# Optimization experiments

Hardware: AMD Instinct MI355X
Metric: run time of the kernel (lower is better)

Reference implementation:

```python
import jax, jax.numpy as jnp
import numpy as np

D_MODEL = 256; D_STATE = 128; EXPAND = 2; HEADDIM = 64
D_INNER = EXPAND * D_MODEL            # 512
NHEADS = D_INNER // HEADDIM           # 8
CONV_DIM = D_INNER + 2 * D_STATE      # 768
D_IN_PROJ = 2 * D_INNER + 2 * D_STATE + NHEADS  # 1288
KCONV = 4
BATCH = 16; SEQ = 1024; CHUNK = 64
EPS = 1e-5


def setup_inputs() -> dict:
    key = jax.random.key(0)
    ks = jax.random.split(key, 8)
    # dt_bias = inverse-softplus of dt ~ U[1e-3, 1e-1] (Mamba2 init)
    dt = jnp.exp(jax.random.uniform(ks[3], (NHEADS,), jnp.float32,
                                    np.log(1e-3), np.log(1e-1)))
    dt_bias = dt + jnp.log(-jnp.expm1(-dt))
    return {
        "u": jax.random.normal(ks[0], (BATCH, SEQ, D_MODEL), jnp.float32),
        "W_in": 0.02 * jax.random.normal(ks[1], (D_MODEL, D_IN_PROJ), jnp.float32),
        "conv_w": 0.2 * jax.random.normal(ks[2], (CONV_DIM, KCONV), jnp.float32),
        "conv_b": jnp.zeros((CONV_DIM,), jnp.float32),
        "dt_bias": dt_bias,
        "A_log": jnp.log(jax.random.uniform(ks[4], (NHEADS,), jnp.float32, 1.0, 16.0)),
        "D": jnp.ones((NHEADS,), jnp.float32),
        "norm_w": jnp.ones((D_INNER,), jnp.float32),
        "W_out": 0.02 * jax.random.normal(ks[5], (D_INNER, D_MODEL), jnp.float32),
    }


def _segsum(x):
    # x: (..., L) -> (..., L, L) lower-triangular cumulative segment sums
    L = x.shape[-1]
    c = jnp.cumsum(x, axis=-1)
    ss = c[..., :, None] - c[..., None, :]
    mask = jnp.tril(jnp.ones((L, L), bool))
    return jnp.where(mask, ss, -jnp.inf)


def _ssd(X, A, Bm, Cm, chunk):
    # Chunked SSD selective scan (Mamba2, ngroups=1).
    # X:(b,t,h,p)  A:(b,t,h)  Bm,Cm:(b,t,n)
    b, t, h, p = X.shape
    nc = t // chunk
    X = X.reshape(b, nc, chunk, h, p)
    A = A.reshape(b, nc, chunk, h).transpose(0, 3, 1, 2)   # (b,h,c,l)
    Bm = Bm.reshape(b, nc, chunk, -1)
    Cm = Cm.reshape(b, nc, chunk, -1)
    A_cs = jnp.cumsum(A, axis=-1)                          # (b,h,c,l)
    Lmat = jnp.exp(_segsum(A))                             # (b,h,c,l,l)
    # within-chunk (diagonal) contribution
    Y_diag = jnp.einsum('bcln,bcsn,bhcls,bcshp->bclhp', Cm, Bm, Lmat, X)
    # per-chunk end states
    decay_states = jnp.exp(A_cs[..., -1:] - A_cs)          # (b,h,c,l)
    states = jnp.einsum('bcln,bhcl,bclhp->bchpn', Bm, decay_states, X)
    # inter-chunk recurrence (vectorized over chunks)
    A_chunk = jnp.pad(A_cs[..., -1], ((0, 0), (0, 0), (1, 0)))
    decay_chunk = jnp.exp(_segsum(A_chunk))                # (b,h,c+1,c+1)
    states = jnp.concatenate([jnp.zeros_like(states[:, :1]), states], axis=1)
    new_states = jnp.einsum('bhzc,bchpn->bzhpn', decay_chunk, states)
    states = new_states[:, :-1]                            # state entering each chunk
    Y_off = jnp.einsum('bcln,bchpn,bhcl->bclhp', Cm, states, jnp.exp(A_cs))
    return (Y_diag + Y_off).reshape(b, t, h, p)


def reference(u, W_in, conv_w, conv_b, dt_bias, A_log, D, norm_w, W_out):
    B, T, _ = u.shape
    zxbcdt = u @ W_in                                      # (B,T,1288)
    z, xBC, dt = jnp.split(zxbcdt, [D_INNER, D_INNER + CONV_DIM], axis=-1)
    # causal depthwise conv1d, kernel KCONV
    xp = jnp.pad(xBC, ((0, 0), (KCONV - 1, 0), (0, 0)))
    kern = conv_w.T[:, None, :]                            # (K,1,C)
    xBC = jax.lax.conv_general_dilated(
        xp, kern, (1,), 'VALID',
        dimension_numbers=('NWC', 'WIO', 'NWC'), feature_group_count=CONV_DIM)
    xBC = jax.nn.silu(xBC + conv_b)
    x, Bc, Cc = jnp.split(xBC, [D_INNER, D_INNER + D_STATE], axis=-1)
    x = x.reshape(B, T, NHEADS, HEADDIM)
    dt = jax.nn.softplus(dt + dt_bias)                     # (B,T,H)
    A = -jnp.exp(A_log)                                    # (H,)
    y = _ssd(x * dt[..., None], dt * A, Bc, Cc, CHUNK)     # (B,T,H,P)
    y = y + D[:, None] * x                                 # skip term
    y = y.reshape(B, T, D_INNER)
    # gated RMSNorm: norm(y * silu(z)) * weight
    g = y * jax.nn.silu(z)
    g = g * jax.lax.rsqrt(jnp.mean(g * g, axis=-1, keepdims=True) + EPS) * norm_w
    return g @ W_out
```

## Files before the change

### kernel.cpp

```cpp
#include <hip/hip_runtime.h>
#include <hip/hip_bf16.h>
#include <math.h>

#define BATCHN  16
#define SEQ     1024
#define DMODEL  256
#define DSTATE  128
#define HEADDIM 64
#define DINNER  512
#define NHEADS  8
#define CONVDIM 768
#define DINPROJ 1288
#define ZXLD    1280
#define KCONV   4
#define NCHUNK  16
#define LCHUNK  64
#define EPSV    1e-5f
#define ROWS    (BATCHN*SEQ)

typedef __attribute__((ext_vector_type(8))) __bf16 bf16x8;
typedef __attribute__((ext_vector_type(4))) float  f32x4;

__device__ inline ushort f2bf(float f) {
    union { float f; uint32_t u; } v; v.f = f;
    uint32_t r = v.u + 0x7fff + ((v.u >> 16) & 1);
    return (ushort)(r >> 16);
}
__device__ inline float bf2f(ushort u) {
    union { uint32_t u; float f; } v; v.u = ((uint32_t)u) << 16;
    return v.f;
}

__global__ __launch_bounds__(256) void transpose_cast2_k(const float* __restrict__ W_in,
                                                         const float* __restrict__ W_out,
                                                         ushort* __restrict__ WtA,
                                                         ushort* __restrict__ WtB) {
    __shared__ float Ts[32][33];
    int bid = blockIdx.x;
    const float* src; ushort* dst; int K, ldsrc, nx;
    if (bid < 320) { src = W_in;  dst = WtA; K = DMODEL; ldsrc = DINPROJ; nx = 40; }
    else { bid -= 320; src = W_out; dst = WtB; K = DINNER; ldsrc = DMODEL; nx = 8; }
    const int n0 = (bid % nx) * 32, k0 = (bid / nx) * 32;
    const int tx = threadIdx.x & 31, ty = threadIdx.x >> 5;
    #pragma unroll
    for (int j = 0; j < 4; ++j) {
        int kl = ty * 4 + j;
        Ts[kl][tx] = src[(size_t)(k0 + kl) * ldsrc + n0 + tx];
    }
    __syncthreads();
    #pragma unroll
    for (int j = 0; j < 4; ++j) {
        int nl = ty * 4 + j;
        dst[(size_t)(n0 + nl) * K + k0 + tx] = f2bf(Ts[tx][nl]);
    }
}

__global__ __launch_bounds__(256) void dt_cast_k(const float* __restrict__ u,
                                                 const float* __restrict__ W_in,
                                                 const float* __restrict__ dt_bias,
                                                 const float* __restrict__ A_log,
                                                 ushort* __restrict__ ubf,
                                                 float* __restrict__ dtb,
                                                 float* __restrict__ adtb) {
    __shared__ float Uld[32][264];
    __shared__ float Ws[DMODEL][NHEADS];
    const int tid = threadIdx.x;
    #pragma unroll
    for (int j = 0; j < 8; ++j) {
        int idx = tid + j * 256;
        Ws[idx >> 3][idx & 7] = W_in[(size_t)(idx >> 3) * DINPROJ + 1280 + (idx & 7)];
    }
    const int row0 = blockIdx.x * 32;
    #pragma unroll
    for (int v = 0; v < 8; ++v) {
        int e = v * 1024 + tid * 4;
        int r = e >> 8, cc = e & 255;
        float4 x = *(const float4*)&u[(size_t)(row0 + r) * DMODEL + cc];
        *(float4*)&Uld[r][cc] = x;
        ushort t4[4];
        t4[0]=f2bf(x.x); t4[1]=f2bf(x.y); t4[2]=f2bf(x.z); t4[3]=f2bf(x.w);
        *(ushort4*)&ubf[(size_t)(row0 + r) * DMODEL + cc] = *(ushort4*)t4;
    }
    __syncthreads();
    const int row = tid >> 3, h = tid & 7;
    float acc = 0.f;
    #pragma unroll 8
    for (int k = 0; k < DMODEL; k += 4) {
        float4 uv = *(const float4*)&Uld[row][k];
        acc += uv.x * Ws[k][h] + uv.y * Ws[k+1][h] + uv.z * Ws[k+2][h] + uv.w * Ws[k+3][h];
    }
    float v = acc + dt_bias[h];
    float dt = (v > 20.f) ? v : log1pf(__expf(v));
    dtb [(size_t)(row0 + row) * NHEADS + h] = dt;
    adtb[(size_t)(row0 + row) * NHEADS + h] = dt * (-__expf(A_log[h]));
}

#define LDSW 72
template<typename CT>
__global__ __launch_bounds__(256) void gemm_bf16(const ushort* __restrict__ A,
                                                 const ushort* __restrict__ Bt,
                                                 CT* __restrict__ C,
                                                 int M, int N, int K, int nx) {
    __shared__ ushort As[128 * LDSW];
    __shared__ ushort Bs[128 * LDSW];
    const int tid  = threadIdx.x;
    const int nwg  = gridDim.x;
    const int work = (blockIdx.x & 7) * (nwg >> 3) + (blockIdx.x >> 3);
    const int m0 = (work / nx) * 128, n0 = (work % nx) * 128;
    const int wid = tid >> 6, lane = tid & 63;
    const int wr = wid >> 1, wc = wid & 1;
    const int r = tid >> 1, kq = tid & 1;
    const int fr = lane & 15, kc = lane >> 4;

    f32x4 acc[4][4];
    #pragma unroll
    for (int i = 0; i < 4; ++i)
        #pragma unroll
        for (int j = 0; j < 4; ++j) acc[i][j] = (f32x4)0.f;

    for (int kt = 0; kt < K; kt += 64) {
        const ushort* ap = &A [(size_t)(m0 + r) * K + kt + kq * 32];
        const ushort* bp = &Bt[(size_t)(n0 + r) * K + kt + kq * 32];
        #pragma unroll
        for (int v = 0; v < 4; ++v) {
            *(uint4*)&As[r * LDSW + kq * 32 + v * 8] = *(const uint4*)(ap + v * 8);
            *(uint4*)&Bs[r * LDSW + kq * 32 + v * 8] = *(const uint4*)(bp + v * 8);
        }
        __syncthreads();
        #pragma unroll
        for (int kk = 0; kk < 2; ++kk) {
            bf16x8 af[4], bfv[4];
            #pragma unroll
            for (int i = 0; i < 4; ++i) {
                af[i]  = *(const bf16x8*)&As[(wr * 64 + i * 16 + fr) * LDSW + kk * 32 + kc * 8];
                bfv[i] = *(const bf16x8*)&Bs[(wc * 64 + i * 16 + fr) * LDSW + kk * 32 + kc * 8];
            }
            #pragma unroll
            for (int i = 0; i < 4; ++i)
                #pragma unroll
                for (int j = 0; j < 4; ++j)
                    acc[i][j] = __builtin_amdgcn_mfma_f32_16x16x32_bf16(af[i], bfv[j], acc[i][j], 0, 0, 0);
        }
        __syncthreads();
    }
    #pragma unroll
    for (int i = 0; i < 4; ++i)
        #pragma unroll
        for (int j = 0; j < 4; ++j)
            #pragma unroll
            for (int q = 0; q < 4; ++q) {
                int rr = m0 + wr * 64 + i * 16 + (lane >> 4) * 4 + q;
                int cc = n0 + wc * 64 + j * 16 + (lane & 15);
                if constexpr (sizeof(CT) == 4) C[(size_t)rr * N + cc] = acc[i][j][q];
                else                           C[(size_t)rr * N + cc] = f2bf(acc[i][j][q]);
            }
}

__global__ __launch_bounds__(256) void conv_silu_k(const ushort* __restrict__ zx,
                                                   const float* __restrict__ cw,
                                                   const float* __restrict__ cb,
                                                   ushort* __restrict__ out) {
    __shared__ float cws[KCONV][CONVDIM];
    __shared__ float cbs[CONVDIM];
    const int tid = threadIdx.x;
    #pragma unroll
    for (int it = 0; it < 3; ++it) {
        int i = tid + it * 256;
        cbs[i] = cb[i];
        #pragma unroll
        for (int k = 0; k < KCONV; ++k) cws[k][i] = cw[i * KCONV + k];
    }
    __syncthreads();

    const int idx = blockIdx.x * 256 + tid;
    const int cg = idx % 96, btq = idx / 96;
    const int c0 = cg * 8;
    const int bt0 = btq * 4;
    const int t0 = bt0 & (SEQ - 1);

    float wv[KCONV][8], bias[8];
    #pragma unroll
    for (int j = 0; j < 8; ++j) bias[j] = cbs[c0 + j];
    #pragma unroll
    for (int k = 0; k < KCONV; ++k) {
        float4 a = *(const float4*)&cws[k][c0];
        float4 b = *(const float4*)&cws[k][c0 + 4];
        wv[k][0] = a.x; wv[k][1] = a.y; wv[k][2] = a.z; wv[k][3] = a.w;
        wv[k][4] = b.x; wv[k][5] = b.y; wv[k][6] = b.z; wv[k][7] = b.w;
    }
    float xr[7][8];
    #pragma unroll
    for (int r = 0; r < 7; ++r) {
        int tt = t0 - 3 + r;
        if (tt >= 0) {
            uint4 v = *(const uint4*)&zx[(size_t)(bt0 - 3 + r) * ZXLD + DINNER + c0];
            const ushort* pv = (const ushort*)&v;
            #pragma unroll
            for (int j = 0; j < 8; ++j) xr[r][j] = bf2f(pv[j]);
        } else {
            #pragma unroll
            for (int j = 0; j < 8; ++j) xr[r][j] = 0.f;
        }
    }
    #pragma unroll
    for (int dt = 0; dt < 4; ++dt) {
        float acc[8];
        #pragma unroll
        for (int j = 0; j < 8; ++j) acc[j] = bias[j];
        #pragma unroll
        for (int k = 0; k < KCONV; ++k)
            #pragma unroll
            for (int j = 0; j < 8; ++j) acc[j] += xr[dt + k][j] * wv[k][j];
        ushort res[8];
        #pragma unroll
        for (int j = 0; j < 8; ++j)
            res[j] = f2bf(acc[j] / (1.f + __expf(-acc[j])));
        *(uint4*)&out[(size_t)(bt0 + dt) * CONVDIM + c0] = *(uint4*)res;
    }
}

#define SLDA 136
#define SLDB 72
__global__ __launch_bounds__(256) void ssd_mfma_k(const ushort* __restrict__ xbc,
                                                  const float* __restrict__ dtb,
                                                  const float* __restrict__ adtb,
                                                  const float* __restrict__ Dp,
                                                  ushort* __restrict__ ybuf,
                                                  ushort* __restrict__ states,
                                                  float* __restrict__ acsbuf,
                                                  float* __restrict__ chunksum) {
    const int c = blockIdx.x, b = blockIdx.y, hgrp = blockIdx.z;
    const int row0 = b * SEQ + c * LCHUNK;
    const int tid = threadIdx.x;
    const int lane = tid & 63, w = tid >> 6;
    const int fr = lane & 15, kc = lane >> 4;

    __shared__ union {
        struct { ushort Bs[64][SLDA]; ushort Cs[64][SLDA]; } p1;
        struct { ushort Ps[64][SLDB]; ushort Xt[64][SLDB]; ushort Xdt[64][SLDB]; } p2;
    } U;
    __shared__ ushort Btr[128][SLDB];
    __shared__ float acs4[4][64];
    __shared__ float dts[4][64];
    __shared__ float decs[4][64];

    {
        const int hh = hgrp * 4 + w;
        float v = adtb[(size_t)(row0 + lane) * NHEADS + hh];
        #pragma unroll
        for (int off = 1; off < 64; off <<= 1) {
            float t = __shfl_up(v, off);
            if (lane >= off) v += t;
        }
        acs4[w][lane] = v;
        float tot = __shfl(v, 63);
        decs[w][lane] = __expf(tot - v);
        acsbuf[(((size_t)b * NCHUNK + c) * NHEADS + hh) * LCHUNK + lane] = v;
        if (lane == 63) chunksum[((size_t)b * NCHUNK + c) * NHEADS + hh] = v;
        dts[w][lane] = dtb[(size_t)(row0 + lane) * NHEADS + hh];
    }
    for (int it = 0; it < 4; ++it) {
        int idx = tid + it * 256;
        int l = idx >> 4, ng = idx & 15;
        const ushort* rp = &xbc[(size_t)(row0 + l) * CONVDIM + DINNER];
        uint4 vb = *(const uint4*)(rp + ng * 8);
        *(uint4*)&U.p1.Bs[l][ng * 8] = vb;
        uint4 vc = *(const uint4*)(rp + DSTATE + ng * 8);
        *(uint4*)&U.p1.Cs[l][ng * 8] = vc;
        const ushort* pv = (const ushort*)&vb;
        #pragma unroll
        for (int j = 0; j < 8; ++j) Btr[ng * 8 + j][l] = pv[j];
    }
    __syncthreads();

    const int wr = w >> 1, wc = w & 1;
    f32x4 accG[2][2];
    #pragma unroll
    for (int i = 0; i < 2; ++i)
        #pragma unroll
        for (int j = 0; j < 2; ++j) accG[i][j] = (f32x4)0.f;
    #pragma unroll
    for (int kt = 0; kt < 4; ++kt) {
        bf16x8 af[2], bfv[2];
        #pragma unroll
        for (int i = 0; i < 2; ++i) af[i]  = *(const bf16x8*)&U.p1.Cs[wr*32 + i*16 + fr][kt*32 + kc*8];
        #pragma unroll
        for (int j = 0; j < 2; ++j) bfv[j] = *(const bf16x8*)&U.p1.Bs[wc*32 + j*16 + fr][kt*32 + kc*8];
        #pragma unroll
        for (int i = 0; i < 2; ++i)
            #pragma unroll
            for (int j = 0; j < 2; ++j)
                accG[i][j] = __builtin_amdgcn_mfma_f32_16x16x32_bf16(af[i], bfv[j], accG[i][j], 0, 0, 0);
    }
    __syncthreads();

    for (int hl = 0; hl < 4; ++hl) {
        const int hh = hgrp * 4 + hl;
        {
            const int p = lane;
            ushort xt[16], xdt[16];
            #pragma unroll
            for (int j = 0; j < 16; ++j) {
                int l = w * 16 + j;
                float xv = bf2f(xbc[(size_t)(row0 + l) * CONVDIM + hh * HEADDIM + p])
                           * dts[hl][l];
                xt[j]  = f2bf(xv);
                xdt[j] = f2bf(xv * decs[hl][l]);
            }
            #pragma unroll
            for (int v = 0; v < 4; ++v) {
                *(ushort4*)&U.p2.Xt [p][w*16 + v*4] = *(ushort4*)&xt[v*4];
                *(ushort4*)&U.p2.Xdt[p][w*16 + v*4] = *(ushort4*)&xdt[v*4];
            }
        }
        #pragma unroll
        for (int i = 0; i < 2; ++i)
            #pragma unroll
            for (int j = 0; j < 2; ++j)
                #pragma unroll
                for (int q = 0; q < 4; ++q) {
                    int l = wr*32 + i*16 + (lane >> 4)*4 + q;
                    int s = wc*32 + j*16 + fr;
                    float v = 0.f;
                    if (s < l)       v = accG[i][j][q] * __expf(acs4[hl][l] - acs4[hl][s]);
                    else if (s == l) v = accG[i][j][q] + Dp[hh] / dts[hl][l];
                    U.p2.Ps[l][s] = f2bf(v);
                }
        __syncthreads();
        {
            f32x4 acc[4];
            #pragma unroll
            for (int j = 0; j < 4; ++j) acc[j] = (f32x4)0.f;
            #pragma unroll
            for (int kt = 0; kt < 2; ++kt) {
                bf16x8 af = *(const bf16x8*)&U.p2.Ps[w*16 + fr][kt*32 + kc*8];
                #pragma unroll
                for (int j = 0; j < 4; ++j) {
                    bf16x8 bfv = *(const bf16x8*)&U.p2.Xt[j*16 + fr][kt*32 + kc*8];
                    acc[j] = __builtin_amdgcn_mfma_f32_16x16x32_bf16(af, bfv, acc[j], 0, 0, 0);
                }
            }
            #pragma unroll
            for (int j = 0; j < 4; ++j)
                #pragma unroll
                for (int q = 0; q < 4; ++q) {
                    int l = w*16 + (lane >> 4)*4 + q;
                    int p = j*16 + fr;
                    ybuf[(size_t)(row0 + l) * DINNER + hh * HEADDIM + p] = f2bf(acc[j][q]);
                }
        }
        {
            f32x4 acc2[4][2];
            #pragma unroll
            for (int mt = 0; mt < 4; ++mt)
                #pragma unroll
                for (int jt = 0; jt < 2; ++jt) acc2[mt][jt] = (f32x4)0.f;
            #pragma unroll
            for (int kt = 0; kt < 2; ++kt) {
                bf16x8 a4[4], b2[2];
                #pragma unroll
                for (int mt = 0; mt < 4; ++mt) a4[mt] = *(const bf16x8*)&U.p2.Xdt[mt*16 + fr][kt*32 + kc*8];
                #pragma unroll
                for (int jt = 0; jt < 2; ++jt) b2[jt] = *(const bf16x8*)&Btr[w*32 + jt*16 + fr][kt*32 + kc*8];
                #pragma unroll
                for (int mt = 0; mt < 4; ++mt)
                    #pragma unroll
                    for (int jt = 0; jt < 2; ++jt)
                        acc2[mt][jt] = __builtin_amdgcn_mfma_f32_16x16x32_bf16(a4[mt], b2[jt], acc2[mt][jt], 0, 0, 0);
            }
            ushort* sb = states + ((((size_t)b * NCHUNK + c) * NHEADS + hh) * HEADDIM) * DSTATE;
            #pragma unroll
            for (int mt = 0; mt < 4; ++mt)
                #pragma unroll
                for (int jt = 0; jt < 2; ++jt)
                    #pragma unroll
                    for (int q = 0; q < 4; ++q) {
                        int p = mt*16 + (lane >> 4)*4 + q;
                        int n = w*32 + jt*16 + fr;
                        sb[(size_t)p * DSTATE + n] = f2bf(acc2[mt][jt][q]);
                    }
        }
        __syncthreads();
    }
}

__global__ __launch_bounds__(256) void scan_k(ushort* __restrict__ states,
                                              const float* __restrict__ chunksum) {
    const int bid = blockIdx.x;
    const int pq = bid & 3, h = (bid >> 2) & 7, b = bid >> 5;
    const int tid = threadIdx.x;
    float pref[8];
    #pragma unroll
    for (int k = 0; k < 8; ++k) pref[k] = 0.f;
    for (int c = 0; c < NCHUNK; ++c) {
        ushort* base = states + (((size_t)b * NCHUNK + c) * NHEADS + h) * (HEADDIM * DSTATE)
                       + pq * 2048 + tid * 8;
        float dec = __expf(chunksum[((size_t)b * NCHUNK + c) * NHEADS + h]);
        uint4 v = *(const uint4*)base;
        const ushort* pv = (const ushort*)&v;
        ushort outv[8];
        #pragma unroll
        for (int j = 0; j < 8; ++j) {
            float cur = bf2f(pv[j]);
            outv[j] = f2bf(pref[j]);
            pref[j] = dec * pref[j] + cur;
        }
        *(uint4*)base = *(uint4*)outv;
    }
}

#define YLDS 520
__global__ __launch_bounds__(256) void yoff_gate_k(const ushort* __restrict__ xbc,
                                                   const ushort* __restrict__ states,
                                                   const float* __restrict__ acsbuf,
                                                   const ushort* __restrict__ ybuf,
                                                   const ushort* __restrict__ zx,
                                                   const float* __restrict__ nw,
                                                   ushort* __restrict__ gbuf) {
    const int c = blockIdx.x, b = blockIdx.y;
    const int row0 = b * SEQ + c * LCHUNK;
    const int tid = threadIdx.x;
    const int lane = tid & 63, w = tid >> 6;
    const int fr = lane & 15, kc = lane >> 4;
    __shared__ ushort Csh[64][SLDA];
    __shared__ ushort Ssh[64][SLDA];
    __shared__ ushort Ys[64][YLDS];
    __shared__ float eah[64];

    for (int it = 0; it < 4; ++it) {
        int idx = tid + it * 256;
        int l = idx >> 4, ng = idx & 15;
        *(uint4*)&Csh[l][ng * 8] =
            *(const uint4*)&xbc[(size_t)(row0 + l) * CONVDIM + DINNER + DSTATE + ng * 8];
    }
    for (int hl = 0; hl < NHEADS; ++hl) {
        __syncthreads();
        const ushort* sb = states + ((((size_t)b * NCHUNK + c) * NHEADS + hl) * HEADDIM) * DSTATE;
        for (int it = 0; it < 4; ++it) {
            int idx = tid + it * 256;
            int p = idx >> 4, ng = idx & 15;
            *(uint4*)&Ssh[p][ng * 8] = *(const uint4*)&sb[(size_t)p * DSTATE + ng * 8];
        }
        if (tid < 64)
            eah[tid] = __expf(acsbuf[(((size_t)b * NCHUNK + c) * NHEADS + hl) * LCHUNK + tid]);
        __syncthreads();
        f32x4 acc[4];
        #pragma unroll
        for (int j = 0; j < 4; ++j) acc[j] = (f32x4)0.f;
        #pragma unroll
        for (int kt = 0; kt < 4; ++kt) {
            bf16x8 af = *(const bf16x8*)&Csh[w*16 + fr][kt*32 + kc*8];
            #pragma unroll
            for (int j = 0; j < 4; ++j) {
                bf16x8 bfv = *(const bf16x8*)&Ssh[j*16 + fr][kt*32 + kc*8];
                acc[j] = __builtin_amdgcn_mfma_f32_16x16x32_bf16(af, bfv, acc[j], 0, 0, 0);
            }
        }
        #pragma unroll
        for (int j = 0; j < 4; ++j)
            #pragma unroll
            for (int q = 0; q < 4; ++q) {
                int l = w*16 + (lane >> 4)*4 + q;
                int p = j*16 + fr;
                float val = bf2f(ybuf[(size_t)(row0 + l) * DINNER + hl * HEADDIM + p])
                            + acc[j][q] * eah[l];
                Ys[l][hl * HEADDIM + p] = f2bf(val);
            }
    }
    __syncthreads();
    float nwv[8];
    #pragma unroll
    for (int j = 0; j < 8; ++j) nwv[j] = nw[lane * 8 + j];
    for (int i = 0; i < 16; ++i) {
        int l = w * 16 + i;
        int row = row0 + l;
        uint4 zv = *(const uint4*)&zx[(size_t)row * ZXLD + lane * 8];
        const ushort* pz = (const ushort*)&zv;
        float g[8], ss = 0.f;
        #pragma unroll
        for (int j = 0; j < 8; ++j) {
            float y = bf2f(Ys[l][lane * 8 + j]);
            float z = bf2f(pz[j]);
            float sz = z / (1.f + __expf(-z));
            g[j] = y * sz;
            ss += g[j] * g[j];
        }
        #pragma unroll
        for (int off = 32; off; off >>= 1) ss += __shfl_xor(ss, off);
        float r = rsqrtf(ss / (float)DINNER + EPSV);
        ushort res[8];
        #pragma unroll
        for (int j = 0; j < 8; ++j) res[j] = f2bf(g[j] * r * nwv[j]);
        *(uint4*)&gbuf[(size_t)row * DINNER + lane * 8] = *(uint4*)res;
    }
}

extern "C" void kernel_launch(void* const* d_in, const int* in_sizes, int n_in,
                              void* d_out, int out_size, void* d_ws, size_t ws_size,
                              hipStream_t stream) {
    const float* u       = (const float*)d_in[0];
    const float* W_in    = (const float*)d_in[1];
    const float* conv_w  = (const float*)d_in[2];
    const float* conv_b  = (const float*)d_in[3];
    const float* dt_bias = (const float*)d_in[4];
    const float* A_log   = (const float*)d_in[5];
    const float* Dp      = (const float*)d_in[6];
    const float* norm_w  = (const float*)d_in[7];
    const float* W_out   = (const float*)d_in[8];
    float* out = (float*)d_out;

    char* p = (char*)d_ws;
    ushort* zx       = (ushort*)p; p += (size_t)ROWS * ZXLD * sizeof(ushort);
    ushort* ybuf     = (ushort*)p; p += (size_t)ROWS * DINNER * sizeof(ushort);
    ushort* gbuf     = (ushort*)p; p += (size_t)ROWS * DINNER * sizeof(ushort);
    ushort* states   = (ushort*)p; p += (size_t)BATCHN * NCHUNK * NHEADS * HEADDIM * DSTATE * sizeof(ushort);
    ushort* xbc      = (ushort*)p; p += (size_t)ROWS * CONVDIM * sizeof(ushort);
    ushort* ubf      = (ushort*)p; p += (size_t)ROWS * DMODEL * sizeof(ushort);
    float*  dtb      = (float*)p;  p += (size_t)ROWS * NHEADS  * sizeof(float);
    float*  adtb     = (float*)p;  p += (size_t)ROWS * NHEADS  * sizeof(float);
    float*  chunksum = (float*)p;  p += (size_t)BATCHN * NCHUNK * NHEADS * sizeof(float);
    float*  acsbuf   = (float*)p;  p += (size_t)BATCHN * NCHUNK * NHEADS * LCHUNK * sizeof(float);
    ushort* WtA      = (ushort*)p; p += (size_t)ZXLD * DMODEL * sizeof(ushort);
    ushort* WtB      = (ushort*)p; p += (size_t)DMODEL * DINNER * sizeof(ushort);

    dt_cast_k<<<ROWS/32, 256, 0, stream>>>(u, W_in, dt_bias, A_log, ubf, dtb, adtb);
    transpose_cast2_k<<<448, 256, 0, stream>>>(W_in, W_out, WtA, WtB);
    gemm_bf16<ushort><<<(ZXLD/128)*(ROWS/128), 256, 0, stream>>>(
        ubf, WtA, zx, ROWS, ZXLD, DMODEL, ZXLD/128);
    conv_silu_k<<<(ROWS/4)*96/256, 256, 0, stream>>>(zx, conv_w, conv_b, xbc);
    ssd_mfma_k<<<dim3(NCHUNK, BATCHN, 2), 256, 0, stream>>>(
        xbc, dtb, adtb, Dp, ybuf, states, acsbuf, chunksum);
    scan_k<<<BATCHN*NHEADS*4, 256, 0, stream>>>(states, chunksum);
    yoff_gate_k<<<dim3(NCHUNK, BATCHN), 256, 0, stream>>>(
        xbc, states, acsbuf, ybuf, zx, norm_w, gbuf);
    gemm_bf16<float><<<(DMODEL/128)*(ROWS/128), 256, 0, stream>>>(
        gbuf, WtB, out, ROWS, DMODEL, DINNER, DMODEL/128);
}
```

Before: 131.4 us.

## Fuse SSD chunk, inter-chunk scan, and state-output into one sequential-chunk kernel

```diff
diff --git a/kernel.cpp b/kernel.cpp
--- a/kernel.cpp
+++ b/kernel.cpp
@@ -221,278 +221,175 @@
 
 #define SLDA 136
 #define SLDB 72
-__global__ __launch_bounds__(256) void ssd_mfma_k(const ushort* __restrict__ xbc,
-                                                  const float* __restrict__ dtb,
-                                                  const float* __restrict__ adtb,
-                                                  const float* __restrict__ Dp,
-                                                  ushort* __restrict__ ybuf,
-                                                  ushort* __restrict__ states,
-                                                  float* __restrict__ acsbuf,
-                                                  float* __restrict__ chunksum) {
-    const int c = blockIdx.x, b = blockIdx.y, hgrp = blockIdx.z;
-    const int row0 = b * SEQ + c * LCHUNK;
+__global__ __launch_bounds__(512) void ssd_fused_k(const ushort* __restrict__ xbc,
+                                                   const float* __restrict__ dtb,
+                                                   const float* __restrict__ adtb,
+                                                   const float* __restrict__ Dp,
+                                                   ushort* __restrict__ ybuf) {
+    const int ph = blockIdx.x, h = blockIdx.y, b = blockIdx.z;
+    const int p0 = ph * 32;
     const int tid = threadIdx.x;
     const int lane = tid & 63, w = tid >> 6;
     const int fr = lane & 15, kc = lane >> 4;
 
-    __shared__ union {
-        struct { ushort Bs[64][SLDA]; ushort Cs[64][SLDA]; } p1;
-        struct { ushort Ps[64][SLDB]; ushort Xt[64][SLDB]; ushort Xdt[64][SLDB]; } p2;
-    } U;
+    __shared__ ushort Bsh[64][SLDA];
+    __shared__ ushort Csh[64][SLDA];
     __shared__ ushort Btr[128][SLDB];
-    __shared__ float acs4[4][64];
-    __shared__ float dts[4][64];
-    __shared__ float decs[4][64];
-
-    {
-        const int hh = hgrp * 4 + w;
-        float v = adtb[(size_t)(row0 + lane) * NHEADS + hh];
-        #pragma unroll
-        for (int off = 1; off < 64; off <<= 1) {
-            float t = __shfl_up(v, off);
-            if (lane >= off) v += t;
-        }
-        acs4[w][lane] = v;
-        float tot = __shfl(v, 63);
-        decs[w][lane] = __expf(tot - v);
-        acsbuf[(((size_t)b * NCHUNK + c) * NHEADS + hh) * LCHUNK + lane] = v;
-        if (lane == 63) chunksum[((size_t)b * NCHUNK + c) * NHEADS + hh] = v;
-        dts[w][lane] = dtb[(size_t)(row0 + lane) * NHEADS + hh];
-    }
-    for (int it = 0; it < 4; ++it) {
-        int idx = tid + it * 256;
-        int l = idx >> 4, ng = idx & 15;
-        const ushort* rp = &xbc[(size_t)(row0 + l) * CONVDIM + DINNER];
-        uint4 vb = *(const uint4*)(rp + ng * 8);
-        *(uint4*)&U.p1.Bs[l][ng * 8] = vb;
-        uint4 vc = *(const uint4*)(rp + DSTATE + ng * 8);
-        *(uint4*)&U.p1.Cs[l][ng * 8] = vc;
-        const ushort* pv = (const ushort*)&vb;
-        #pragma unroll
-        for (int j = 0; j < 8; ++j) Btr[ng * 8 + j][l] = pv[j];
-    }
+    __shared__ ushort Ps [64][SLDB];
+    __shared__ ushort Xt [32][SLDB];
+    __shared__ ushort Xdt[32][SLDB];
+    __shared__ ushort Spl[32][SLDA];
+    __shared__ float acs_s[64], dts_s[64], decs_s[64];
+
+    const float Dh = Dp[h];
+    { int p = tid >> 4, ng = tid & 15;
+      uint4 z; z.x = z.y = z.z = z.w = 0u;
+      *(uint4*)&Spl[p][ng * 8] = z; }
+    const int mt = w & 1, nt0 = (w >> 1) * 2;
+    f32x4 Sp[2];
+    Sp[0] = (f32x4)0.f; Sp[1] = (f32x4)0.f;
     __syncthreads();
 
-    const int wr = w >> 1, wc = w & 1;
-    f32x4 accG[2][2];
-    #pragma unroll
-    for (int i = 0; i < 2; ++i)
-        #pragma unroll
-        for (int j = 0; j < 2; ++j) accG[i][j] = (f32x4)0.f;
-    #pragma unroll
-    for (int kt = 0; kt < 4; ++kt) {
-        bf16x8 af[2], bfv[2];
-        #pragma unroll
-        for (int i = 0; i < 2; ++i) af[i]  = *(const bf16x8*)&U.p1.Cs[wr*32 + i*16 + fr][kt*32 + kc*8];
-        #pragma unroll
-        for (int j = 0; j < 2; ++j) bfv[j] = *(const bf16x8*)&U.p1.Bs[wc*32 + j*16 + fr][kt*32 + kc*8];
-        #pragma unroll
-        for (int i = 0; i < 2; ++i)
-            #pragma unroll
-            for (int j = 0; j < 2; ++j)
-                accG[i][j] = __builtin_amdgcn_mfma_f32_16x16x32_bf16(af[i], bfv[j], accG[i][j], 0, 0, 0);
-    }
-    __syncthreads();
-
-    for (int hl = 0; hl < 4; ++hl) {
-        const int hh = hgrp * 4 + hl;
-        {
-            const int p = lane;
-            ushort xt[16], xdt[16];
-            #pragma unroll
-            for (int j = 0; j < 16; ++j) {
-                int l = w * 16 + j;
-                float xv = bf2f(xbc[(size_t)(row0 + l) * CONVDIM + hh * HEADDIM + p])
-                           * dts[hl][l];
-                xt[j]  = f2bf(xv);
-                xdt[j] = f2bf(xv * decs[hl][l]);
-            }
-            #pragma unroll
-            for (int v = 0; v < 4; ++v) {
-                *(ushort4*)&U.p2.Xt [p][w*16 + v*4] = *(ushort4*)&xt[v*4];
-                *(ushort4*)&U.p2.Xdt[p][w*16 + v*4] = *(ushort4*)&xdt[v*4];
-            }
-        }
-        #pragma unroll
-        for (int i = 0; i < 2; ++i)
-            #pragma unroll
-            for (int j = 0; j < 2; ++j)
-                #pragma unroll
-                for (int q = 0; q < 4; ++q) {
-                    int l = wr*32 + i*16 + (lane >> 4)*4 + q;
-                    int s = wc*32 + j*16 + fr;
-                    float v = 0.f;
-                    if (s < l)       v = accG[i][j][q] * __expf(acs4[hl][l] - acs4[hl][s]);
-                    else if (s == l) v = accG[i][j][q] + Dp[hh] / dts[hl][l];
-                    U.p2.Ps[l][s] = f2bf(v);
-                }
+    for (int c = 0; c < NCHUNK; ++c) {
+        const int row0 = b * SEQ + c * LCHUNK;
+        if (w == 0) {
+            float v = adtb[(size_t)(row0 + lane) * NHEADS + h];
+            #pragma unroll
+            for (int off = 1; off < 64; off <<= 1) {
+                float t = __shfl_up(v, off);
+                if (lane >= off) v += t;
+            }
+            acs_s[lane] = v;
+            float tot = __shfl(v, 63);
+            decs_s[lane] = __expf(tot - v);
+            dts_s[lane] = dtb[(size_t)(row0 + lane) * NHEADS + h];
+        }
+        #pragma unroll
+        for (int it = 0; it < 2; ++it) {
+            int idx = tid + it * 512;
+            int l = idx >> 4, ng = idx & 15;
+            const ushort* rp = &xbc[(size_t)(row0 + l) * CONVDIM + DINNER];
+            uint4 vb = *(const uint4*)(rp + ng * 8);
+            *(uint4*)&Bsh[l][ng * 8] = vb;
+            uint4 vc = *(const uint4*)(rp + DSTATE + ng * 8);
+            *(uint4*)&Csh[l][ng * 8] = vc;
+            const ushort* pv = (const ushort*)&vb;
+            #pragma unroll
+            for (int j = 0; j < 8; ++j) Btr[ng * 8 + j][l] = pv[j];
+        }
         __syncthreads();
-        {
-            f32x4 acc[4];
-            #pragma unroll
-            for (int j = 0; j < 4; ++j) acc[j] = (f32x4)0.f;
-            #pragma unroll
-            for (int kt = 0; kt < 2; ++kt) {
-                bf16x8 af = *(const bf16x8*)&U.p2.Ps[w*16 + fr][kt*32 + kc*8];
-                #pragma unroll
-                for (int j = 0; j < 4; ++j) {
-                    bf16x8 bfv = *(const bf16x8*)&U.p2.Xt[j*16 + fr][kt*32 + kc*8];
-                    acc[j] = __builtin_amdgcn_mfma_f32_16x16x32_bf16(af, bfv, acc[j], 0, 0, 0);
-                }
-            }
-            #pragma unroll
-            for (int j = 0; j < 4; ++j)
-                #pragma unroll
-                for (int q = 0; q < 4; ++q) {
-                    int l = w*16 + (lane >> 4)*4 + q;
-                    int p = j*16 + fr;
-                    ybuf[(size_t)(row0 + l) * DINNER + hh * HEADDIM + p] = f2bf(acc[j][q]);
-                }
-        }
-        {
-            f32x4 acc2[4][2];
-            #pragma unroll
-            for (int mt = 0; mt < 4; ++mt)
-                #pragma unroll
-                for (int jt = 0; jt < 2; ++jt) acc2[mt][jt] = (f32x4)0.f;
-            #pragma unroll
-            for (int kt = 0; kt < 2; ++kt) {
-                bf16x8 a4[4], b2[2];
-                #pragma unroll
-                for (int mt = 0; mt < 4; ++mt) a4[mt] = *(const bf16x8*)&U.p2.Xdt[mt*16 + fr][kt*32 + kc*8];
-                #pragma unroll
-                for (int jt = 0; jt < 2; ++jt) b2[jt] = *(const bf16x8*)&Btr[w*32 + jt*16 + fr][kt*32 + kc*8];
-                #pragma unroll
-                for (int mt = 0; mt < 4; ++mt)
-                    #pragma unroll
-                    for (int jt = 0; jt < 2; ++jt)
-                        acc2[mt][jt] = __builtin_amdgcn_mfma_f32_16x16x32_bf16(a4[mt], b2[jt], acc2[mt][jt], 0, 0, 0);
-            }
-            ushort* sb = states + ((((size_t)b * NCHUNK + c) * NHEADS + hh) * HEADDIM) * DSTATE;
-            #pragma unroll
-            for (int mt = 0; mt < 4; ++mt)
-                #pragma unroll
-                for (int jt = 0; jt < 2; ++jt)
-                    #pragma unroll
-                    for (int q = 0; q < 4; ++q) {
-                        int p = mt*16 + (lane >> 4)*4 + q;
-                        int n = w*32 + jt*16 + fr;
-                        sb[(size_t)p * DSTATE + n] = f2bf(acc2[mt][jt][q]);
-                    }
+
+        const int gi = w >> 1, gj0 = (w & 1) * 2;
+        f32x4 accG[2];
+        accG[0] = (f32x4)0.f; accG[1] = (f32x4)0.f;
+        #pragma unroll
+        for (int kt = 0; kt < 4; ++kt) {
+            bf16x8 af = *(const bf16x8*)&Csh[gi*16 + fr][kt*32 + kc*8];
+            #pragma unroll
+            for (int jj = 0; jj < 2; ++jj) {
+                bf16x8 bfv = *(const bf16x8*)&Bsh[(gj0+jj)*16 + fr][kt*32 + kc*8];
+                accG[jj] = __builtin_amdgcn_mfma_f32_16x16x32_bf16(af, bfv, accG[jj], 0, 0, 0);
+            }
+        }
+        #pragma unroll
+        for (int jj = 0; jj < 2; ++jj)
+            #pragma unroll
+            for (int q = 0; q < 4; ++q) {
+                int l = gi*16 + (lane >> 4)*4 + q;
+                int s = (gj0+jj)*16 + fr;
+                float v = 0.f;
+                if (s < l)       v = accG[jj][q] * __expf(acs_s[l] - acs_s[s]);
+                else if (s == l) v = accG[jj][q] + Dh / dts_s[l];
+                Ps[l][s] = f2bf(v);
+            }
+        if (tid < 256) {
+            int l = tid >> 2, gg = tid & 3;
+            uint4 xv4 = *(const uint4*)&xbc[(size_t)(row0 + l) * CONVDIM
+                                            + h * HEADDIM + p0 + gg * 8];
+            const ushort* pv = (const ushort*)&xv4;
+            float dt_l = dts_s[l], dec_l = decs_s[l];
+            #pragma unroll
+            for (int j = 0; j < 8; ++j) {
+                float xv = bf2f(pv[j]) * dt_l;
+                Xt [gg*8 + j][l] = f2bf(xv);
+                Xdt[gg*8 + j][l] = f2bf(xv * dec_l);
+            }
+        }
+        const int yi = w >> 1, yj = w & 1;
+        f32x4 accO = (f32x4)0.f;
+        #pragma unroll
+        for (int kt = 0; kt < 4; ++kt) {
+            bf16x8 af  = *(const bf16x8*)&Csh[yi*16 + fr][kt*32 + kc*8];
+            bf16x8 bfv = *(const bf16x8*)&Spl[yj*16 + fr][kt*32 + kc*8];
+            accO = __builtin_amdgcn_mfma_f32_16x16x32_bf16(af, bfv, accO, 0, 0, 0);
         }
         __syncthreads();
-    }
-}
-
-__global__ __launch_bounds__(256) void scan_k(ushort* __restrict__ states,
-                                              const float* __restrict__ chunksum) {
-    const int bid = blockIdx.x;
-    const int pq = bid & 3, h = (bid >> 2) & 7, b = bid >> 5;
-    const int tid = threadIdx.x;
-    float pref[8];
-    #pragma unroll
-    for (int k = 0; k < 8; ++k) pref[k] = 0.f;
-    for (int c = 0; c < NCHUNK; ++c) {
-        ushort* base = states + (((size_t)b * NCHUNK + c) * NHEADS + h) * (HEADDIM * DSTATE)
-                       + pq * 2048 + tid * 8;
-        float dec = __expf(chunksum[((size_t)b * NCHUNK + c) * NHEADS + h]);
-        uint4 v = *(const uint4*)base;
-        const ushort* pv = (const ushort*)&v;
-        ushort outv[8];
-        #pragma unroll
-        for (int j = 0; j < 8; ++j) {
-            float cur = bf2f(pv[j]);
-            outv[j] = f2bf(pref[j]);
-            pref[j] = dec * pref[j] + cur;
-        }
-        *(uint4*)base = *(uint4*)outv;
-    }
-}
-
-#define YLDS 520
-__global__ __launch_bounds__(256) void yoff_gate_k(const ushort* __restrict__ xbc,
-                                                   const ushort* __restrict__ states,
-                                                   const float* __restrict__ acsbuf,
-                                                   const ushort* __restrict__ ybuf,
+
+        f32x4 accD = (f32x4)0.f;
+        #pragma unroll
+        for (int kt = 0; kt < 2; ++kt) {
+            bf16x8 af  = *(const bf16x8*)&Ps[yi*16 + fr][kt*32 + kc*8];
+            bf16x8 bfv = *(const bf16x8*)&Xt[yj*16 + fr][kt*32 + kc*8];
+            accD = __builtin_amdgcn_mfma_f32_16x16x32_bf16(af, bfv, accD, 0, 0, 0);
+        }
+        #pragma unroll
+        for (int q = 0; q < 4; ++q) {
+            int l = yi*16 + (lane >> 4)*4 + q;
+            float ea = __expf(acs_s[l]);
+            ybuf[(size_t)(row0 + l) * DINNER + h * HEADDIM + p0 + yj*16 + fr]
+                = f2bf(accD[q] + accO[q] * ea);
+        }
+        f32x4 accS[2];
+        accS[0] = (f32x4)0.f; accS[1] = (f32x4)0.f;
+        #pragma unroll
+        for (int kt = 0; kt < 2; ++kt) {
+            bf16x8 af = *(const bf16x8*)&Xdt[mt*16 + fr][kt*32 + kc*8];
+            #pragma unroll
+            for (int jt = 0; jt < 2; ++jt) {
+                bf16x8 bfv = *(const bf16x8*)&Btr[(nt0+jt)*16 + fr][kt*32 + kc*8];
+                accS[jt] = __builtin_amdgcn_mfma_f32_16x16x32_bf16(af, bfv, accS[jt], 0, 0, 0);
+            }
+        }
+        const float decC = __expf(acs_s[63]);
+        #pragma unroll
+        for (int jt = 0; jt < 2; ++jt)
+            #pragma unroll
+            for (int q = 0; q < 4; ++q) {
+                Sp[jt][q] = decC * Sp[jt][q] + accS[jt][q];
+                int p = mt*16 + (lane >> 4)*4 + q;
+                int n = (nt0+jt)*16 + fr;
+                Spl[p][n] = f2bf(Sp[jt][q]);
+            }
+        __syncthreads();
+    }
+}
+
+__global__ __launch_bounds__(256) void gate_norm_k(const ushort* __restrict__ ybuf,
                                                    const ushort* __restrict__ zx,
                                                    const float* __restrict__ nw,
                                                    ushort* __restrict__ gbuf) {
-    const int c = blockIdx.x, b = blockIdx.y;
-    const int row0 = b * SEQ + c * LCHUNK;
-    const int tid = threadIdx.x;
-    const int lane = tid & 63, w = tid >> 6;
-    const int fr = lane & 15, kc = lane >> 4;
-    __shared__ ushort Csh[64][SLDA];
-    __shared__ ushort Ssh[64][SLDA];
-    __shared__ ushort Ys[64][YLDS];
-    __shared__ float eah[64];
-
-    for (int it = 0; it < 4; ++it) {
-        int idx = tid + it * 256;
-        int l = idx >> 4, ng = idx & 15;
-        *(uint4*)&Csh[l][ng * 8] =
-            *(const uint4*)&xbc[(size_t)(row0 + l) * CONVDIM + DINNER + DSTATE + ng * 8];
-    }
-    for (int hl = 0; hl < NHEADS; ++hl) {
-        __syncthreads();
-        const ushort* sb = states + ((((size_t)b * NCHUNK + c) * NHEADS + hl) * HEADDIM) * DSTATE;
-        for (int it = 0; it < 4; ++it) {
-            int idx = tid + it * 256;
-            int p = idx >> 4, ng = idx & 15;
-            *(uint4*)&Ssh[p][ng * 8] = *(const uint4*)&sb[(size_t)p * DSTATE + ng * 8];
-        }
-        if (tid < 64)
-            eah[tid] = __expf(acsbuf[(((size_t)b * NCHUNK + c) * NHEADS + hl) * LCHUNK + tid]);
-        __syncthreads();
-        f32x4 acc[4];
-        #pragma unroll
-        for (int j = 0; j < 4; ++j) acc[j] = (f32x4)0.f;
-        #pragma unroll
-        for (int kt = 0; kt < 4; ++kt) {
-            bf16x8 af = *(const bf16x8*)&Csh[w*16 + fr][kt*32 + kc*8];
-            #pragma unroll
-            for (int j = 0; j < 4; ++j) {
-                bf16x8 bfv = *(const bf16x8*)&Ssh[j*16 + fr][kt*32 + kc*8];
-                acc[j] = __builtin_amdgcn_mfma_f32_16x16x32_bf16(af, bfv, acc[j], 0, 0, 0);
-            }
-        }
-        #pragma unroll
-        for (int j = 0; j < 4; ++j)
-            #pragma unroll
-            for (int q = 0; q < 4; ++q) {
-                int l = w*16 + (lane >> 4)*4 + q;
-                int p = j*16 + fr;
-                float val = bf2f(ybuf[(size_t)(row0 + l) * DINNER + hl * HEADDIM + p])
-                            + acc[j][q] * eah[l];
-                Ys[l][hl * HEADDIM + p] = f2bf(val);
-            }
-    }
-    __syncthreads();
-    float nwv[8];
-    #pragma unroll
-    for (int j = 0; j < 8; ++j) nwv[j] = nw[lane * 8 + j];
-    for (int i = 0; i < 16; ++i) {
-        int l = w * 16 + i;
-        int row = row0 + l;
-        uint4 zv = *(const uint4*)&zx[(size_t)row * ZXLD + lane * 8];
-        const ushort* pz = (const ushort*)&zv;
-        float g[8], ss = 0.f;
-        #pragma unroll
-        for (int j = 0; j < 8; ++j) {
-            float y = bf2f(Ys[l][lane * 8 + j]);
-            float z = bf2f(pz[j]);
-            float sz = z / (1.f + __expf(-z));
-            g[j] = y * sz;
-            ss += g[j] * g[j];
-        }
-        #pragma unroll
-        for (int off = 32; off; off >>= 1) ss += __shfl_xor(ss, off);
-        float r = rsqrtf(ss / (float)DINNER + EPSV);
-        ushort res[8];
-        #pragma unroll
-        for (int j = 0; j < 8; ++j) res[j] = f2bf(g[j] * r * nwv[j]);
-        *(uint4*)&gbuf[(size_t)row * DINNER + lane * 8] = *(uint4*)res;
-    }
+    const int row  = blockIdx.x * 4 + (threadIdx.x >> 6);
+    const int lane = threadIdx.x & 63;
+    uint4 yv = *(const uint4*)&ybuf[(size_t)row * DINNER + lane * 8];
+    uint4 zv = *(const uint4*)&zx[(size_t)row * ZXLD + lane * 8];
+    const ushort* py = (const ushort*)&yv;
+    const ushort* pz = (const ushort*)&zv;
+    float g[8], ss = 0.f;
+    #pragma unroll
+    for (int j = 0; j < 8; ++j) {
+        float y = bf2f(py[j]);
+        float z = bf2f(pz[j]);
+        float sz = z / (1.f + __expf(-z));
+        g[j] = y * sz;
+        ss += g[j] * g[j];
+    }
+    #pragma unroll
+    for (int off = 32; off; off >>= 1) ss += __shfl_xor(ss, off);
+    float r = rsqrtf(ss / (float)DINNER + EPSV);
+    ushort res[8];
+    #pragma unroll
+    for (int j = 0; j < 8; ++j) res[j] = f2bf(g[j] * r * nw[lane * 8 + j]);
+    *(uint4*)&gbuf[(size_t)row * DINNER + lane * 8] = *(uint4*)res;
 }
 
 extern "C" void kernel_launch(void* const* d_in, const int* in_sizes, int n_in,
@@ -513,13 +410,10 @@
     ushort* zx       = (ushort*)p; p += (size_t)ROWS * ZXLD * sizeof(ushort);
     ushort* ybuf     = (ushort*)p; p += (size_t)ROWS * DINNER * sizeof(ushort);
     ushort* gbuf     = (ushort*)p; p += (size_t)ROWS * DINNER * sizeof(ushort);
-    ushort* states   = (ushort*)p; p += (size_t)BATCHN * NCHUNK * NHEADS * HEADDIM * DSTATE * sizeof(ushort);
     ushort* xbc      = (ushort*)p; p += (size_t)ROWS * CONVDIM * sizeof(ushort);
     ushort* ubf      = (ushort*)p; p += (size_t)ROWS * DMODEL * sizeof(ushort);
     float*  dtb      = (float*)p;  p += (size_t)ROWS * NHEADS  * sizeof(float);
     float*  adtb     = (float*)p;  p += (size_t)ROWS * NHEADS  * sizeof(float);
-    float*  chunksum = (float*)p;  p += (size_t)BATCHN * NCHUNK * NHEADS * sizeof(float);
-    float*  acsbuf   = (float*)p;  p += (size_t)BATCHN * NCHUNK * NHEADS * LCHUNK * sizeof(float);
     ushort* WtA      = (ushort*)p; p += (size_t)ZXLD * DMODEL * sizeof(ushort);
     ushort* WtB      = (ushort*)p; p += (size_t)DMODEL * DINNER * sizeof(ushort);
 
@@ -528,11 +422,9 @@
     gemm_bf16<ushort><<<(ZXLD/128)*(ROWS/128), 256, 0, stream>>>(
         ubf, WtA, zx, ROWS, ZXLD, DMODEL, ZXLD/128);
     conv_silu_k<<<(ROWS/4)*96/256, 256, 0, stream>>>(zx, conv_w, conv_b, xbc);
-    ssd_mfma_k<<<dim3(NCHUNK, BATCHN, 2), 256, 0, stream>>>(
-        xbc, dtb, adtb, Dp, ybuf, states, acsbuf, chunksum);
-    scan_k<<<BATCHN*NHEADS*4, 256, 0, stream>>>(states, chunksum);
-    yoff_gate_k<<<dim3(NCHUNK, BATCHN), 256, 0, stream>>>(
-        xbc, states, acsbuf, ybuf, zx, norm_w, gbuf);
+    ssd_fused_k<<<dim3(2, NHEADS, BATCHN), 512, 0, stream>>>(
+        xbc, dtb, adtb, Dp, ybuf);
+    gate_norm_k<<<ROWS/4, 256, 0, stream>>>(ybuf, zx, norm_w, gbuf);
     gemm_bf16<float><<<(DMODEL/128)*(ROWS/128), 256, 0, stream>>>(
         gbuf, WtB, out, ROWS, DMODEL, DINNER, DMODEL/128);
 }
```

Result: slower. 149.2 us (+13.5%).

## Fuse causal conv+SiLU into in-projection GEMM epilogue with boundary fix kernel

Applied to the files above, without the earlier changes.

```diff
diff --git a/kernel.cpp b/kernel.cpp
--- a/kernel.cpp
+++ b/kernel.cpp
@@ -96,13 +96,20 @@
 }
 
 #define LDSW 72
-template<typename CT>
+#define TILEW 136
+template<typename CT, bool FCONV>
 __global__ __launch_bounds__(256) void gemm_bf16(const ushort* __restrict__ A,
                                                  const ushort* __restrict__ Bt,
                                                  CT* __restrict__ C,
-                                                 int M, int N, int K, int nx) {
-    __shared__ ushort As[128 * LDSW];
-    __shared__ ushort Bs[128 * LDSW];
+                                                 int M, int N, int K, int nx,
+                                                 const float* __restrict__ cw,
+                                                 const float* __restrict__ cb,
+                                                 ushort* __restrict__ xbc) {
+    __shared__ ushort LB[2 * 128 * LDSW];
+    __shared__ float cwsl[128][4];
+    __shared__ float cbl[128];
+    ushort* As = LB;
+    ushort* Bs = LB + 128 * LDSW;
     const int tid  = threadIdx.x;
     const int nwg  = gridDim.x;
     const int work = (blockIdx.x & 7) * (nwg >> 3) + (blockIdx.x >> 3);
@@ -111,6 +118,19 @@
     const int wr = wid >> 1, wc = wid & 1;
     const int r = tid >> 1, kq = tid & 1;
     const int fr = lane & 15, kc = lane >> 4;
+    const bool doconv = FCONV && (n0 >= DINNER);
+
+    if constexpr (FCONV) {
+        if (doconv) {
+            int cbase = n0 - DINNER;
+            if (tid < 128) cbl[tid] = cb[cbase + tid];
+            #pragma unroll
+            for (int s = 0; s < 2; ++s) {
+                int flat = tid + s * 256;
+                cwsl[flat >> 2][flat & 3] = cw[cbase * 4 + flat];
+            }
+        }
+    }
 
     f32x4 acc[4][4];
     #pragma unroll
@@ -143,23 +163,70 @@
         }
         __syncthreads();
     }
+    ushort (*Tile)[TILEW] = (ushort (*)[TILEW])LB;
     #pragma unroll
     for (int i = 0; i < 4; ++i)
         #pragma unroll
         for (int j = 0; j < 4; ++j)
             #pragma unroll
             for (int q = 0; q < 4; ++q) {
-                int rr = m0 + wr * 64 + i * 16 + (lane >> 4) * 4 + q;
-                int cc = n0 + wc * 64 + j * 16 + (lane & 15);
-                if constexpr (sizeof(CT) == 4) C[(size_t)rr * N + cc] = acc[i][j][q];
-                else                           C[(size_t)rr * N + cc] = f2bf(acc[i][j][q]);
-            }
-}
-
-__global__ __launch_bounds__(256) void conv_silu_k(const ushort* __restrict__ zx,
-                                                   const float* __restrict__ cw,
-                                                   const float* __restrict__ cb,
-                                                   ushort* __restrict__ out) {
+                int rl = wr * 64 + i * 16 + (lane >> 4) * 4 + q;
+                int cl = wc * 64 + j * 16 + (lane & 15);
+                if constexpr (sizeof(CT) == 4) C[(size_t)(m0 + rl) * N + n0 + cl] = acc[i][j][q];
+                else {
+                    ushort bv = f2bf(acc[i][j][q]);
+                    C[(size_t)(m0 + rl) * N + n0 + cl] = bv;
+                    if (doconv) Tile[rl][cl] = bv;
+                }
+            }
+    if constexpr (FCONV) {
+        if (!doconv) return;
+        __syncthreads();
+        const int cg = tid & 15, rg = tid >> 4;
+        const int c0l = cg * 8;
+        float wk[KCONV][8], bias[8];
+        #pragma unroll
+        for (int k = 0; k < KCONV; ++k)
+            #pragma unroll
+            for (int j = 0; j < 8; ++j) wk[k][j] = cwsl[c0l + j][k];
+        #pragma unroll
+        for (int j = 0; j < 8; ++j) bias[j] = cbl[c0l + j];
+        const int start = (rg == 0) ? 3 : rg * 8;
+        float win[3][8];
+        #pragma unroll
+        for (int s = 0; s < 3; ++s) {
+            uint4 v = *(const uint4*)&Tile[start - 3 + s][c0l];
+            const ushort* pv = (const ushort*)&v;
+            #pragma unroll
+            for (int j = 0; j < 8; ++j) win[s][j] = bf2f(pv[j]);
+        }
+        for (int rr = start; rr < rg * 8 + 8; ++rr) {
+            uint4 v = *(const uint4*)&Tile[rr][c0l];
+            const ushort* pv = (const ushort*)&v;
+            float cur[8], a8[8];
+            #pragma unroll
+            for (int j = 0; j < 8; ++j) {
+                cur[j] = bf2f(pv[j]);
+                a8[j] = bias[j] + wk[0][j]*win[0][j] + wk[1][j]*win[1][j]
+                                + wk[2][j]*win[2][j] + wk[3][j]*cur[j];
+            }
+            #pragma unroll
+            for (int j = 0; j < 8; ++j) {
+                win[0][j] = win[1][j]; win[1][j] = win[2][j]; win[2][j] = cur[j];
+            }
+            ushort res[8];
+            #pragma unroll
+            for (int j = 0; j < 8; ++j)
+                res[j] = f2bf(a8[j] / (1.f + __expf(-a8[j])));
+            *(uint4*)&xbc[(size_t)(m0 + rr) * CONVDIM + (n0 - DINNER) + c0l] = *(uint4*)res;
+        }
+    }
+}
+
+__global__ __launch_bounds__(256) void conv_fix_k(const ushort* __restrict__ zx,
+                                                  const float* __restrict__ cw,
+                                                  const float* __restrict__ cb,
+                                                  ushort* __restrict__ xbc) {
     __shared__ float cws[KCONV][CONVDIM];
     __shared__ float cbs[CONVDIM];
     const int tid = threadIdx.x;
@@ -171,51 +238,29 @@
         for (int k = 0; k < KCONV; ++k) cws[k][i] = cw[i * KCONV + k];
     }
     __syncthreads();
-
-    const int idx = blockIdx.x * 256 + tid;
-    const int cg = idx % 96, btq = idx / 96;
-    const int c0 = cg * 8;
-    const int bt0 = btq * 4;
-    const int t0 = bt0 & (SEQ - 1);
-
-    float wv[KCONV][8], bias[8];
-    #pragma unroll
-    for (int j = 0; j < 8; ++j) bias[j] = cbs[c0 + j];
-    #pragma unroll
-    for (int k = 0; k < KCONV; ++k) {
-        float4 a = *(const float4*)&cws[k][c0];
-        float4 b = *(const float4*)&cws[k][c0 + 4];
-        wv[k][0] = a.x; wv[k][1] = a.y; wv[k][2] = a.z; wv[k][3] = a.w;
-        wv[k][4] = b.x; wv[k][5] = b.y; wv[k][6] = b.z; wv[k][7] = b.w;
-    }
-    float xr[7][8];
-    #pragma unroll
-    for (int r = 0; r < 7; ++r) {
-        int tt = t0 - 3 + r;
-        if (tt >= 0) {
-            uint4 v = *(const uint4*)&zx[(size_t)(bt0 - 3 + r) * ZXLD + DINNER + c0];
+    const int m0 = blockIdx.x * 128;
+    for (int it = tid; it < 288; it += 256) {
+        int l = it / 96, cg = it % 96;
+        int c0 = cg * 8;
+        int bt = m0 + l;
+        int t = bt & (SEQ - 1);
+        float a8[8];
+        #pragma unroll
+        for (int j = 0; j < 8; ++j) a8[j] = cbs[c0 + j];
+        #pragma unroll
+        for (int k = 0; k < KCONV; ++k) {
+            int tt = t - 3 + k;
+            if (tt < 0) continue;
+            uint4 v = *(const uint4*)&zx[(size_t)(bt - 3 + k) * ZXLD + DINNER + c0];
             const ushort* pv = (const ushort*)&v;
             #pragma unroll
-            for (int j = 0; j < 8; ++j) xr[r][j] = bf2f(pv[j]);
-        } else {
-            #pragma unroll
-            for (int j = 0; j < 8; ++j) xr[r][j] = 0.f;
-        }
-    }
-    #pragma unroll
-    for (int dt = 0; dt < 4; ++dt) {
-        float acc[8];
-        #pragma unroll
-        for (int j = 0; j < 8; ++j) acc[j] = bias[j];
-        #pragma unroll
-        for (int k = 0; k < KCONV; ++k)
-            #pragma unroll
-            for (int j = 0; j < 8; ++j) acc[j] += xr[dt + k][j] * wv[k][j];
+            for (int j = 0; j < 8; ++j) a8[j] += bf2f(pv[j]) * cws[k][c0 + j];
+        }
         ushort res[8];
         #pragma unroll
         for (int j = 0; j < 8; ++j)
-            res[j] = f2bf(acc[j] / (1.f + __expf(-acc[j])));
-        *(uint4*)&out[(size_t)(bt0 + dt) * CONVDIM + c0] = *(uint4*)res;
+            res[j] = f2bf(a8[j] / (1.f + __expf(-a8[j])));
+        *(uint4*)&xbc[(size_t)bt * CONVDIM + c0] = *(uint4*)res;
     }
 }
 
@@ -229,7 +274,7 @@
                                                   ushort* __restrict__ states,
                                                   float* __restrict__ acsbuf,
                                                   float* __restrict__ chunksum) {
-    const int c = blockIdx.x, b = blockIdx.y, hgrp = blockIdx.z;
+    const int hgrp = blockIdx.x, c = blockIdx.y, b = blockIdx.z;
     const int row0 = b * SEQ + c * LCHUNK;
     const int tid = threadIdx.x;
     const int lane = tid & 63, w = tid >> 6;
@@ -525,14 +570,14 @@
 
     dt_cast_k<<<ROWS/32, 256, 0, stream>>>(u, W_in, dt_bias, A_log, ubf, dtb, adtb);
     transpose_cast2_k<<<448, 256, 0, stream>>>(W_in, W_out, WtA, WtB);
-    gemm_bf16<ushort><<<(ZXLD/128)*(ROWS/128), 256, 0, stream>>>(
-        ubf, WtA, zx, ROWS, ZXLD, DMODEL, ZXLD/128);
-    conv_silu_k<<<(ROWS/4)*96/256, 256, 0, stream>>>(zx, conv_w, conv_b, xbc);
-    ssd_mfma_k<<<dim3(NCHUNK, BATCHN, 2), 256, 0, stream>>>(
+    gemm_bf16<ushort, true><<<(ZXLD/128)*(ROWS/128), 256, 0, stream>>>(
+        ubf, WtA, zx, ROWS, ZXLD, DMODEL, ZXLD/128, conv_w, conv_b, xbc);
+    conv_fix_k<<<ROWS/128, 256, 0, stream>>>(zx, conv_w, conv_b, xbc);
+    ssd_mfma_k<<<dim3(2, NCHUNK, BATCHN), 256, 0, stream>>>(
         xbc, dtb, adtb, Dp, ybuf, states, acsbuf, chunksum);
     scan_k<<<BATCHN*NHEADS*4, 256, 0, stream>>>(states, chunksum);
     yoff_gate_k<<<dim3(NCHUNK, BATCHN), 256, 0, stream>>>(
         xbc, states, acsbuf, ybuf, zx, norm_w, gbuf);
-    gemm_bf16<float><<<(DMODEL/128)*(ROWS/128), 256, 0, stream>>>(
-        gbuf, WtB, out, ROWS, DMODEL, DINNER, DMODEL/128);
-}
+    gemm_bf16<float, false><<<(DMODEL/128)*(ROWS/128), 256, 0, stream>>>(
+        gbuf, WtB, out, ROWS, DMODEL, DINNER, DMODEL/128, nullptr, nullptr, nullptr);
+}
```

After: 142.0 us. 1.08x slower.
